# Optimization experiments

Measured on AMD Instinct MI355X. Metric: run time of the kernel, lower is better.

## Reference

```python
import jax, jax.numpy as jnp
import numpy as np

N = 100000      # nodes
E = 1600000     # directed edges
F_IN = 128      # node feature dim
H = 128         # hidden dim
C = 16          # classes


def setup_inputs() -> dict:
    key = jax.random.key(0)
    ks = jax.random.split(key, 8)
    s = 1.0 / np.sqrt(H)
    return {
        "x": jax.random.normal(ks[0], (N, F_IN), dtype=jnp.float32),
        "edge_index": jax.random.randint(ks[1], (2, E), 0, N, dtype=jnp.int32),
        "W1": jax.random.normal(ks[2], (F_IN, H), dtype=jnp.float32) * s,
        "b1": jnp.zeros((H,), jnp.float32),
        "W2": jax.random.normal(ks[3], (H, H), dtype=jnp.float32) * s,
        "b2": jnp.zeros((H,), jnp.float32),
        "W3": jax.random.normal(ks[4], (H, H), dtype=jnp.float32) * s,
        "b3": jnp.zeros((H,), jnp.float32),
        "Wfc": jax.random.normal(ks[5], (H, C), dtype=jnp.float32) * s,
        "bfc": jnp.zeros((C,), jnp.float32),
    }


def _gcn_conv(x, W, b, src, dst, norm):
    # x' = b + scatter_add over edges of norm * (x @ W)[src] into dst
    h = x @ W                                   # [N, H] dense GEMM
    msg = h[src] * norm[:, None]                # [E+N, H] gather + scale
    out = jax.ops.segment_sum(msg, dst, num_segments=N)  # scatter-add
    return out + b


def reference(x, edge_index, W1, b1, W2, b2, W3, b3, Wfc, bfc):
    loops = jnp.arange(N, dtype=edge_index.dtype)
    src = jnp.concatenate([edge_index[0], loops])   # [E+N] with self-loops
    dst = jnp.concatenate([edge_index[1], loops])
    # symmetric normalization deg^{-1/2}[src] * deg^{-1/2}[dst] (PyG default)
    deg = jax.ops.segment_sum(jnp.ones_like(dst, dtype=x.dtype), dst, num_segments=N)
    dinv = jax.lax.rsqrt(deg)                       # deg >= 1 due to self-loops
    norm = dinv[src] * dinv[dst]

    h = jax.nn.elu(_gcn_conv(x, W1, b1, src, dst, norm))   # dropout is identity in eval
    h = jax.nn.elu(_gcn_conv(h, W2, b2, src, dst, norm))
    h = jax.nn.elu(_gcn_conv(h, W3, b3, src, dst, norm))
    logits = h @ Wfc + bfc                                  # [N, C]
    return jax.nn.log_softmax(logits, axis=-1)
```

## Files before the change

### kernel.cpp

```cpp
#include <hip/hip_runtime.h>
#include <math.h>

#define HDIM 128
#define CDIM 16
#define CAP 48
#define ASTR 136
#define NBINS 256
#define TILE 4096
#define F2SPLIT 4

typedef unsigned short u16;
typedef unsigned int u32;
typedef __attribute__((ext_vector_type(8))) short short8;
typedef __attribute__((ext_vector_type(4))) float f32x4;

__device__ inline u16 f2bf(float f) {
  u32 u = __float_as_uint(f);
  u += 0x7fffu + ((u >> 16) & 1u);
  return (u16)(u >> 16);
}
__device__ inline float bf_lo(u32 p) { return __uint_as_float(p << 16); }
__device__ inline float bf_hi(u32 p) { return __uint_as_float(p & 0xffff0000u); }
__device__ inline u32 pack2(float a, float b) {
  return (u32)f2bf(a) | ((u32)f2bf(b) << 16);
}
__device__ inline void addp(float2* a, uint4 g) {
  a[0].x += bf_lo(g.x); a[0].y += bf_hi(g.x);
  a[1].x += bf_lo(g.y); a[1].y += bf_hi(g.y);
  a[2].x += bf_lo(g.z); a[2].y += bf_hi(g.z);
  a[3].x += bf_lo(g.w); a[3].y += bf_hi(g.w);
}


__global__ __launch_bounds__(256) void bin_kernel(const int* __restrict__ ei,
                                                  int* __restrict__ cursor,
                                                  int2* __restrict__ bins,
                                                  int binCap, int E, int npb, int nbE,
                                                  int* __restrict__ deg, int N,
                                                  const float* __restrict__ W0,
                                                  const float* __restrict__ W1,
                                                  const float* __restrict__ W2,
                                                  u16* __restrict__ Wt) {
  int tid = threadIdx.x;
  if (blockIdx.x >= nbE) {
    int t = (blockIdx.x - nbE) * 256 + tid;
    int which = t >> 14, idx = t & 16383;
    int n = idx >> 7, k = idx & 127;
    const float* W = which == 0 ? W0 : (which == 1 ? W1 : W2);
    Wt[(size_t)which * HDIM * HDIM + n * HDIM + k] = f2bf(W[k * HDIM + n]);
    return;
  }
  {
    int i = blockIdx.x * 256 + tid;
    if (i < N) deg[i] = 0;
  }
  __shared__ int2 eds[TILE];
  __shared__ int base[NBINS], rank[NBINS], hist[NBINS];
  int t0 = blockIdx.x * TILE;
  int n = min(TILE, E - t0);
  for (int i = tid; i < NBINS; i += 256) { hist[i] = 0; rank[i] = 0; }
  __syncthreads();
  for (int i = tid; i < n; i += 256) {
    int s = ei[t0 + i];
    int d = ei[E + t0 + i];
    eds[i] = make_int2(d, s);
    atomicAdd(&hist[d / npb], 1);
  }
  __syncthreads();
  for (int i = tid; i < NBINS; i += 256) {
    int h = hist[i];
    base[i] = h ? atomicAdd(&cursor[i], h) : 0;
  }
  __syncthreads();
  for (int i = tid; i < n; i += 256) {
    int2 e = eds[i];
    int b = e.x / npb;
    int r = base[b] + atomicAdd(&rank[b], 1);
    if (r < binCap) bins[(size_t)b * binCap + r] = e;
  }
}

__global__ __launch_bounds__(256) void fill2_kernel(const int2* __restrict__ bins,
                                                    const int* __restrict__ cursor,
                                                    int binCap, int* __restrict__ deg,
                                                    int* __restrict__ csr) {
  int b = blockIdx.x & (NBINS - 1);
  int part = blockIdx.x >> 8;
  int cnt = min(cursor[b], binCap);
  const int2* eb = bins + (size_t)b * binCap;
  for (int i = part * 256 + threadIdx.x; i < cnt; i += 256 * F2SPLIT) {
    int2 e = eb[i];
    int p = atomicAdd(&deg[e.x], 1);
    if (p < CAP) csr[(size_t)e.x * CAP + p] = e.y;
  }
}


template <bool FP32IN>
__global__ __launch_bounds__(256) void gemm_k(const void* __restrict__ Xv,
                                              const u16* __restrict__ Wt,
                                              const int* __restrict__ deg,
                                              u16* __restrict__ G, int N) {
  __shared__ u16 As[64 * ASTR];
  __shared__ u16 Wsm[128 * ASTR];
  int tid = threadIdx.x;
  int row0 = blockIdx.x * 64;

  {
    int r = tid >> 2, c = tid & 3;
    int rg = row0 + r;
    if (rg >= N) rg = N - 1;
    uint4* dst = (uint4*)(As + r * ASTR + c * 32);
    if (FP32IN) {
      const float4* src = (const float4*)((const float*)Xv + (size_t)rg * HDIM + c * 32);
#pragma unroll
      for (int j = 0; j < 4; ++j) {
        float4 a = src[2 * j], b = src[2 * j + 1];
        uint4 o;
        o.x = pack2(a.x, a.y); o.y = pack2(a.z, a.w);
        o.z = pack2(b.x, b.y); o.w = pack2(b.z, b.w);
        dst[j] = o;
      }
    } else {
      const uint4* src = (const uint4*)((const u16*)Xv + (size_t)rg * HDIM + c * 32);
      dst[0] = src[0]; dst[1] = src[1]; dst[2] = src[2]; dst[3] = src[3];
    }
  }
  {
    int r = tid >> 1, h = tid & 1;
    const uint4* src = (const uint4*)(Wt + r * HDIM + h * 64);
    uint4* dst = (uint4*)(Wsm + r * ASTR + h * 64);
#pragma unroll
    for (int i = 0; i < 8; ++i) dst[i] = src[i];
  }
  __syncthreads();

  int w = tid >> 6;
  int l = tid & 63;
  int m = l & 15, q = l >> 4;

  f32x4 acc[8];
#pragma unroll
  for (int i = 0; i < 8; ++i) acc[i] = (f32x4){0.f, 0.f, 0.f, 0.f};

#pragma unroll
  for (int kc = 0; kc < 4; ++kc) {
    short8 af = *(const short8*)(As + (w * 16 + m) * ASTR + kc * 32 + q * 8);
#pragma unroll
    for (int nt = 0; nt < 8; ++nt) {
      short8 bfr = *(const short8*)(Wsm + (nt * 16 + m) * ASTR + kc * 32 + q * 8);
      acc[nt] = __builtin_amdgcn_mfma_f32_16x16x32_bf16(af, bfr, acc[nt], 0, 0, 0);
    }
  }
  __syncthreads();

  float dv[4];
#pragma unroll
  for (int r = 0; r < 4; ++r) {
    int rg = row0 + w * 16 + q * 4 + r;
    dv[r] = rsqrtf((float)(deg[rg < N ? rg : N - 1] + 1));
  }
#pragma unroll
  for (int nt = 0; nt < 8; ++nt)
#pragma unroll
    for (int r = 0; r < 4; ++r)
      As[(w * 16 + q * 4 + r) * ASTR + nt * 16 + m] = f2bf(acc[nt][r] * dv[r]);
  __syncthreads();

  {
    int r = tid >> 2, c = tid & 3;
    int rg = row0 + r;
    if (rg < N) {
      uint4* dst = (uint4*)(G + (size_t)rg * HDIM + c * 32);
      const uint4* src = (const uint4*)(As + r * ASTR + c * 32);
      dst[0] = src[0]; dst[1] = src[1]; dst[2] = src[2]; dst[3] = src[3];
    }
  }
}


__device__ inline void gather_node(const u16* __restrict__ G, const int* __restrict__ deg,
                                   const int* __restrict__ csr,
                                   const float4* __restrict__ b4, int node, int l, float* v) {
  float2 a[4];
  {
    uint4 s = *(const uint4*)(G + (size_t)node * HDIM + l * 8);
    a[0] = make_float2(bf_lo(s.x), bf_hi(s.x));
    a[1] = make_float2(bf_lo(s.y), bf_hi(s.y));
    a[2] = make_float2(bf_lo(s.z), bf_hi(s.z));
    a[3] = make_float2(bf_lo(s.w), bf_hi(s.w));
  }
  int dfull = deg[node];
  int d = min(dfull, CAP);
  const int* row = csr + (size_t)node * CAP;
  int i = 0;
  for (; i + 4 <= d; i += 4) {
    int u0 = row[i], u1 = row[i + 1], u2 = row[i + 2], u3 = row[i + 3];
    uint4 g0 = *(const uint4*)(G + (size_t)u0 * HDIM + l * 8);
    uint4 g1 = *(const uint4*)(G + (size_t)u1 * HDIM + l * 8);
    uint4 g2 = *(const uint4*)(G + (size_t)u2 * HDIM + l * 8);
    uint4 g3 = *(const uint4*)(G + (size_t)u3 * HDIM + l * 8);
    addp(a, g0); addp(a, g1); addp(a, g2); addp(a, g3);
  }
  for (; i < d; ++i) {
    uint4 g = *(const uint4*)(G + (size_t)row[i] * HDIM + l * 8);
    addp(a, g);
  }
  float dvn = rsqrtf((float)(dfull + 1));
  float4 b0 = b4[l * 2], b1 = b4[l * 2 + 1];
  v[0] = fmaf(dvn, a[0].x, b0.x); v[1] = fmaf(dvn, a[0].y, b0.y);
  v[2] = fmaf(dvn, a[1].x, b0.z); v[3] = fmaf(dvn, a[1].y, b0.w);
  v[4] = fmaf(dvn, a[2].x, b1.x); v[5] = fmaf(dvn, a[2].y, b1.y);
  v[6] = fmaf(dvn, a[3].x, b1.z); v[7] = fmaf(dvn, a[3].y, b1.w);
#pragma unroll
  for (int j = 0; j < 8; ++j) v[j] = v[j] > 0.f ? v[j] : expm1f(v[j]);
}


__global__ __launch_bounds__(256) void agg_bf(const u16* __restrict__ G,
                                              const int* __restrict__ deg,
                                              const int* __restrict__ csr,
                                              const float* __restrict__ b,
                                              u16* __restrict__ out, int N) {
  int node = blockIdx.x * 16 + (threadIdx.x >> 4);
  if (node >= N) return;
  int l = threadIdx.x & 15;
  float v[8];
  gather_node(G, deg, csr, (const float4*)b, node, l, v);
  uint4 o;
  o.x = pack2(v[0], v[1]); o.y = pack2(v[2], v[3]);
  o.z = pack2(v[4], v[5]); o.w = pack2(v[6], v[7]);
  *(uint4*)(out + (size_t)node * HDIM + l * 8) = o;
}


__global__ __launch_bounds__(256) void agg_fc(const u16* __restrict__ G,
                                              const int* __restrict__ deg,
                                              const int* __restrict__ csr,
                                              const float* __restrict__ b,
                                              const float* __restrict__ Wfc,
                                              const float* __restrict__ bfc,
                                              float* __restrict__ out, int N) {
  __shared__ u16 As[16 * ASTR];
  __shared__ float Wl[HDIM * CDIM];
  int tid = threadIdx.x;
  for (int i = tid; i < HDIM * CDIM; i += 256) Wl[i] = Wfc[i];

  int node0 = blockIdx.x * 16;
  int lr = tid >> 4, l = tid & 15;
  int node = node0 + lr;
  if (node < N) {
    float v[8];
    gather_node(G, deg, csr, (const float4*)b, node, l, v);
    uint4 o;
    o.x = pack2(v[0], v[1]); o.y = pack2(v[2], v[3]);
    o.z = pack2(v[4], v[5]); o.w = pack2(v[6], v[7]);
    *(uint4*)(As + lr * ASTR + l * 8) = o;
  }
  __syncthreads();

  int rg = node0 + lr;
  if (rg >= N) return;
  int c = l;
  const u16* hrow = As + lr * ASTR;
  float acc = bfc[c];
#pragma unroll 4
  for (int k8 = 0; k8 < 16; ++k8) {
    uint4 g = *(const uint4*)(hrow + k8 * 8);
    const float* wk = Wl + (k8 * 8) * CDIM + c;
    acc = fmaf(bf_lo(g.x), wk[0 * CDIM], acc);
    acc = fmaf(bf_hi(g.x), wk[1 * CDIM], acc);
    acc = fmaf(bf_lo(g.y), wk[2 * CDIM], acc);
    acc = fmaf(bf_hi(g.y), wk[3 * CDIM], acc);
    acc = fmaf(bf_lo(g.z), wk[4 * CDIM], acc);
    acc = fmaf(bf_hi(g.z), wk[5 * CDIM], acc);
    acc = fmaf(bf_lo(g.w), wk[6 * CDIM], acc);
    acc = fmaf(bf_hi(g.w), wk[7 * CDIM], acc);
  }
  float mx = acc;
  for (int off = 8; off >= 1; off >>= 1) mx = fmaxf(mx, __shfl_xor(mx, off, 16));
  float ex = expf(acc - mx);
  float ssum = ex;
  for (int off = 8; off >= 1; off >>= 1) ssum += __shfl_xor(ssum, off, 16);
  out[(size_t)rg * CDIM + c] = (acc - mx) - logf(ssum);
}


extern "C" void kernel_launch(void* const* d_in, const int* in_sizes, int n_in,
                              void* d_out, int out_size, void* d_ws, size_t ws_size,
                              hipStream_t stream) {
  const float* x   = (const float*)d_in[0];
  const int*   ei  = (const int*)d_in[1];
  const float* W1  = (const float*)d_in[2];
  const float* b1  = (const float*)d_in[3];
  const float* W2  = (const float*)d_in[4];
  const float* b2  = (const float*)d_in[5];
  const float* W3  = (const float*)d_in[6];
  const float* b3  = (const float*)d_in[7];
  const float* Wfc = (const float*)d_in[8];
  const float* bfc = (const float*)d_in[9];

  const int N = in_sizes[0] / HDIM;
  const int E = in_sizes[1] / 2;
  const int npb = (N + NBINS - 1) / NBINS;
  const int binCap = (E + NBINS - 1) / NBINS + 1024;
  const int nbE = (E + TILE - 1) / TILE;
  const int nbW = 3 * HDIM * HDIM / 256;

  char* ws = (char*)d_ws;
  size_t off = 0;
  auto alloc = [&](size_t bytes) -> void* {
    void* p = ws + off;
    off += (bytes + 511) & ~(size_t)511;
    return p;
  };
  int*   deg    = (int*)alloc((size_t)N * 4);
  int*   cursor = (int*)alloc((size_t)NBINS * 4);
  int*   csr    = (int*)alloc((size_t)N * CAP * 4);
  int2*  bins   = (int2*)alloc((size_t)NBINS * binCap * 8);
  u16*   Wt     = (u16*)alloc((size_t)3 * HDIM * HDIM * 2);
  u16*   A      = (u16*)alloc((size_t)N * HDIM * 2);
  u16*   B      = (u16*)alloc((size_t)N * HDIM * 2);

  hipMemsetAsync(cursor, 0, (size_t)NBINS * 4, stream);
  bin_kernel<<<nbE + nbW, 256, 0, stream>>>(ei, cursor, bins, binCap, E, npb, nbE, deg, N, W1,
                                            W2, W3, Wt);
  fill2_kernel<<<NBINS * F2SPLIT, 256, 0, stream>>>(bins, cursor, binCap, deg, csr);

  int grid64 = (N + 63) / 64;
  int grid16 = (N + 15) / 16;
  gemm_k<true><<<grid64, 256, 0, stream>>>(x, Wt, deg, A, N);
  agg_bf<<<grid16, 256, 0, stream>>>(A, deg, csr, b1, B, N);
  gemm_k<false><<<grid64, 256, 0, stream>>>(B, Wt + HDIM * HDIM, deg, A, N);
  agg_bf<<<grid16, 256, 0, stream>>>(A, deg, csr, b2, B, N);
  gemm_k<false><<<grid64, 256, 0, stream>>>(B, Wt + 2 * HDIM * HDIM, deg, A, N);
  agg_fc<<<grid16, 256, 0, stream>>>(A, deg, csr, b3, Wfc, bfc, (float*)d_out, N);
}
```

Before: 417.3 us.

## Use 32 lanes per node in aggregation with padded CSR and shuffled indices

Aggregation now assigns 32 lanes per node instead of 16. The two 16-lane halves each process alternate neighbors and are combined with an xor-shuffle reduction. CSR rows are padded to multiples of 16 with a sentinel index pointing at a zeroed extra row, which removes the tail loop. Neighbor indices are loaded once per lane and broadcast by shuffle. Packed f32 adds go through inline asm. This raises memory-level parallelism per node in exchange for wasted loads on padding, an extra pad kernel and memsets, and half the lanes idling in the epilogue.

```diff
diff --git a/kernel.cpp b/kernel.cpp
--- a/kernel.cpp
+++ b/kernel.cpp
@@ -13,6 +13,7 @@
 typedef unsigned int u32;
 typedef __attribute__((ext_vector_type(8))) short short8;
 typedef __attribute__((ext_vector_type(4))) float f32x4;
+typedef __attribute__((ext_vector_type(2))) float f32x2;
 
 __device__ inline u16 f2bf(float f) {
   u32 u = __float_as_uint(f);
@@ -24,11 +25,19 @@
 __device__ inline u32 pack2(float a, float b) {
   return (u32)f2bf(a) | ((u32)f2bf(b) << 16);
 }
-__device__ inline void addp(float2* a, uint4 g) {
-  a[0].x += bf_lo(g.x); a[0].y += bf_hi(g.x);
-  a[1].x += bf_lo(g.y); a[1].y += bf_hi(g.y);
-  a[2].x += bf_lo(g.z); a[2].y += bf_hi(g.z);
-  a[3].x += bf_lo(g.w); a[3].y += bf_hi(g.w);
+
+__device__ inline void acc_word(f32x2& acc, u32 w) {
+  f32x2 x;
+  x.x = __uint_as_float(w << 16);
+  x.y = __uint_as_float(w & 0xffff0000u);
+  asm("v_pk_add_f32 %0, %1, %2" : "=v"(acc) : "v"(x), "v"(acc));
+}
+__device__ inline f32x2 xor16_add(f32x2 a) {
+  f32x2 o;
+  o.x = __shfl_xor(a.x, 16, 32);
+  o.y = __shfl_xor(a.y, 16, 32);
+  asm("v_pk_add_f32 %0, %1, %2" : "=v"(a) : "v"(o), "v"(a));
+  return a;
 }
 
 
@@ -95,6 +104,16 @@
   }
 }
 
+__global__ __launch_bounds__(256) void pad_kernel(const int* __restrict__ deg,
+                                                  int* __restrict__ csr, int N) {
+  int n = blockIdx.x * 256 + threadIdx.x;
+  if (n >= N) return;
+  int d = min(deg[n], CAP);
+  int dp = (d + 15) & ~15;
+  int* row = csr + (size_t)n * CAP;
+  for (int i = d; i < dp; ++i) row[i] = N;
+}
+
 
 template <bool FP32IN>
 __global__ __launch_bounds__(256) void gemm_k(const void* __restrict__ Xv,
@@ -179,39 +198,50 @@
 }
 
 
-__device__ inline void gather_node(const u16* __restrict__ G, const int* __restrict__ deg,
-                                   const int* __restrict__ csr,
-                                   const float4* __restrict__ b4, int node, int l, float* v) {
-  float2 a[4];
-  {
-    uint4 s = *(const uint4*)(G + (size_t)node * HDIM + l * 8);
-    a[0] = make_float2(bf_lo(s.x), bf_hi(s.x));
-    a[1] = make_float2(bf_lo(s.y), bf_hi(s.y));
-    a[2] = make_float2(bf_lo(s.z), bf_hi(s.z));
-    a[3] = make_float2(bf_lo(s.w), bf_hi(s.w));
-  }
+__device__ inline void gather32(const u16* __restrict__ G, const int* __restrict__ deg,
+                                const int* __restrict__ csr,
+                                const float4* __restrict__ b4, int node, int cl, float* v) {
+  const char* Gb = (const char*)G;
+  int l = cl & 15, g = cl >> 4;
+  uint4 sr = make_uint4(0, 0, 0, 0);
+  if (g == 0) sr = *(const uint4*)(Gb + ((size_t)node << 8) + (l << 4));
+  f32x2 p0, p1, p2, p3;
+  p0.x = bf_lo(sr.x); p0.y = bf_hi(sr.x);
+  p1.x = bf_lo(sr.y); p1.y = bf_hi(sr.y);
+  p2.x = bf_lo(sr.z); p2.y = bf_hi(sr.z);
+  p3.x = bf_lo(sr.w); p3.y = bf_hi(sr.w);
+
   int dfull = deg[node];
   int d = min(dfull, CAP);
+  int dp = (d + 15) & ~15;
   const int* row = csr + (size_t)node * CAP;
-  int i = 0;
-  for (; i + 4 <= d; i += 4) {
-    int u0 = row[i], u1 = row[i + 1], u2 = row[i + 2], u3 = row[i + 3];
-    uint4 g0 = *(const uint4*)(G + (size_t)u0 * HDIM + l * 8);
-    uint4 g1 = *(const uint4*)(G + (size_t)u1 * HDIM + l * 8);
-    uint4 g2 = *(const uint4*)(G + (size_t)u2 * HDIM + l * 8);
-    uint4 g3 = *(const uint4*)(G + (size_t)u3 * HDIM + l * 8);
-    addp(a, g0); addp(a, g1); addp(a, g2); addp(a, g3);
-  }
-  for (; i < d; ++i) {
-    uint4 g = *(const uint4*)(G + (size_t)row[i] * HDIM + l * 8);
-    addp(a, g);
-  }
+  int i0 = row[cl];
+  int i1 = (cl < 16) ? row[32 + cl] : 0;
+
+#define GLD(u) (*(const uint4*)(Gb + (((u32)(u)) << 8) + (l << 4)))
+#define AW(gv) { acc_word(p0, gv.x); acc_word(p1, gv.y); acc_word(p2, gv.z); acc_word(p3, gv.w); }
+  for (int k = 0; k < dp; k += 16) {
+    int s = k < 32 ? i0 : i1;
+    int bl = (k < 32 ? k : 0) + g;
+    int u0 = __shfl(s, bl + 0, 32), u1 = __shfl(s, bl + 2, 32);
+    int u2 = __shfl(s, bl + 4, 32), u3 = __shfl(s, bl + 6, 32);
+    int u4 = __shfl(s, bl + 8, 32), u5 = __shfl(s, bl + 10, 32);
+    int u6 = __shfl(s, bl + 12, 32), u7 = __shfl(s, bl + 14, 32);
+    uint4 g0 = GLD(u0), g1 = GLD(u1), g2 = GLD(u2), g3 = GLD(u3);
+    uint4 g4 = GLD(u4), g5 = GLD(u5), g6 = GLD(u6), g7 = GLD(u7);
+    AW(g0) AW(g1) AW(g2) AW(g3) AW(g4) AW(g5) AW(g6) AW(g7)
+  }
+#undef AW
+#undef GLD
+  p0 = xor16_add(p0); p1 = xor16_add(p1);
+  p2 = xor16_add(p2); p3 = xor16_add(p3);
+
   float dvn = rsqrtf((float)(dfull + 1));
   float4 b0 = b4[l * 2], b1 = b4[l * 2 + 1];
-  v[0] = fmaf(dvn, a[0].x, b0.x); v[1] = fmaf(dvn, a[0].y, b0.y);
-  v[2] = fmaf(dvn, a[1].x, b0.z); v[3] = fmaf(dvn, a[1].y, b0.w);
-  v[4] = fmaf(dvn, a[2].x, b1.x); v[5] = fmaf(dvn, a[2].y, b1.y);
-  v[6] = fmaf(dvn, a[3].x, b1.z); v[7] = fmaf(dvn, a[3].y, b1.w);
+  v[0] = fmaf(dvn, p0.x, b0.x); v[1] = fmaf(dvn, p0.y, b0.y);
+  v[2] = fmaf(dvn, p1.x, b0.z); v[3] = fmaf(dvn, p1.y, b0.w);
+  v[4] = fmaf(dvn, p2.x, b1.x); v[5] = fmaf(dvn, p2.y, b1.y);
+  v[6] = fmaf(dvn, p3.x, b1.z); v[7] = fmaf(dvn, p3.y, b1.w);
 #pragma unroll
   for (int j = 0; j < 8; ++j) v[j] = v[j] > 0.f ? v[j] : expm1f(v[j]);
 }
@@ -222,15 +252,17 @@
                                               const int* __restrict__ csr,
                                               const float* __restrict__ b,
                                               u16* __restrict__ out, int N) {
-  int node = blockIdx.x * 16 + (threadIdx.x >> 4);
+  int node = blockIdx.x * 8 + (threadIdx.x >> 5);
   if (node >= N) return;
-  int l = threadIdx.x & 15;
+  int cl = threadIdx.x & 31;
   float v[8];
-  gather_node(G, deg, csr, (const float4*)b, node, l, v);
-  uint4 o;
-  o.x = pack2(v[0], v[1]); o.y = pack2(v[2], v[3]);
-  o.z = pack2(v[4], v[5]); o.w = pack2(v[6], v[7]);
-  *(uint4*)(out + (size_t)node * HDIM + l * 8) = o;
+  gather32(G, deg, csr, (const float4*)b, node, cl, v);
+  if (cl < 16) {
+    uint4 o;
+    o.x = pack2(v[0], v[1]); o.y = pack2(v[2], v[3]);
+    o.z = pack2(v[4], v[5]); o.w = pack2(v[6], v[7]);
+    *(uint4*)(out + (size_t)node * HDIM + cl * 8) = o;
+  }
 }
 
 
@@ -241,27 +273,30 @@
                                               const float* __restrict__ Wfc,
                                               const float* __restrict__ bfc,
                                               float* __restrict__ out, int N) {
-  __shared__ u16 As[16 * ASTR];
+  __shared__ u16 As[8 * ASTR];
   __shared__ float Wl[HDIM * CDIM];
   int tid = threadIdx.x;
   for (int i = tid; i < HDIM * CDIM; i += 256) Wl[i] = Wfc[i];
 
-  int node0 = blockIdx.x * 16;
-  int lr = tid >> 4, l = tid & 15;
-  int node = node0 + lr;
+  int node0 = blockIdx.x * 8;
+  int nr = tid >> 5, cl = tid & 31, l = cl & 15;
+  int node = node0 + nr;
   if (node < N) {
     float v[8];
-    gather_node(G, deg, csr, (const float4*)b, node, l, v);
-    uint4 o;
-    o.x = pack2(v[0], v[1]); o.y = pack2(v[2], v[3]);
-    o.z = pack2(v[4], v[5]); o.w = pack2(v[6], v[7]);
-    *(uint4*)(As + lr * ASTR + l * 8) = o;
-  }
-  __syncthreads();
-
+    gather32(G, deg, csr, (const float4*)b, node, cl, v);
+    if (cl < 16) {
+      uint4 o;
+      o.x = pack2(v[0], v[1]); o.y = pack2(v[2], v[3]);
+      o.z = pack2(v[4], v[5]); o.w = pack2(v[6], v[7]);
+      *(uint4*)(As + nr * ASTR + l * 8) = o;
+    }
+  }
+  __syncthreads();
+
+  int lr = tid >> 4, c = tid & 15;
+  if (lr >= 8) return;
   int rg = node0 + lr;
   if (rg >= N) return;
-  int c = l;
   const u16* hrow = As + lr * ASTR;
   float acc = bfc[c];
 #pragma unroll 4
@@ -319,20 +354,23 @@
   int*   csr    = (int*)alloc((size_t)N * CAP * 4);
   int2*  bins   = (int2*)alloc((size_t)NBINS * binCap * 8);
   u16*   Wt     = (u16*)alloc((size_t)3 * HDIM * HDIM * 2);
-  u16*   A      = (u16*)alloc((size_t)N * HDIM * 2);
-  u16*   B      = (u16*)alloc((size_t)N * HDIM * 2);
+  u16*   A      = (u16*)alloc((size_t)(N + 1) * HDIM * 2);
+  u16*   B      = (u16*)alloc((size_t)(N + 1) * HDIM * 2);
 
   hipMemsetAsync(cursor, 0, (size_t)NBINS * 4, stream);
+  hipMemsetAsync(A + (size_t)N * HDIM, 0, HDIM * 2, stream);
+  hipMemsetAsync(B + (size_t)N * HDIM, 0, HDIM * 2, stream);
   bin_kernel<<<nbE + nbW, 256, 0, stream>>>(ei, cursor, bins, binCap, E, npb, nbE, deg, N, W1,
                                             W2, W3, Wt);
   fill2_kernel<<<NBINS * F2SPLIT, 256, 0, stream>>>(bins, cursor, binCap, deg, csr);
+  pad_kernel<<<(N + 255) / 256, 256, 0, stream>>>(deg, csr, N);
 
   int grid64 = (N + 63) / 64;
-  int grid16 = (N + 15) / 16;
+  int grid8 = (N + 7) / 8;
   gemm_k<true><<<grid64, 256, 0, stream>>>(x, Wt, deg, A, N);
-  agg_bf<<<grid16, 256, 0, stream>>>(A, deg, csr, b1, B, N);
+  agg_bf<<<grid8, 256, 0, stream>>>(A, deg, csr, b1, B, N);
   gemm_k<false><<<grid64, 256, 0, stream>>>(B, Wt + HDIM * HDIM, deg, A, N);
-  agg_bf<<<grid16, 256, 0, stream>>>(A, deg, csr, b2, B, N);
+  agg_bf<<<grid8, 256, 0, stream>>>(A, deg, csr, b2, B, N);
   gemm_k<false><<<grid64, 256, 0, stream>>>(B, Wt + 2 * HDIM * HDIM, deg, A, N);
-  agg_fc<<<grid16, 256, 0, stream>>>(A, deg, csr, b3, Wfc, bfc, (float*)d_out, N);
-}
+  agg_fc<<<grid8, 256, 0, stream>>>(A, deg, csr, b3, Wfc, bfc, (float*)d_out, N);
+}
```

Measured after the change: 411.4 us. About the same (-1.4%).
